# Kernel tuning notes

Measured on AMD Instinct MI355X. Metric: run time of the kernel, lower is better.

## Reference

```python
import jax, jax.numpy as jnp
import numpy as np

N, T, L = 4, 2048, 2048
DQIN, DFEAT, DQK, DV = 32, 34, 64, 64  # modality feat=34 -> V input = 34-2 = 32, K input = last col


def _sorted_timeline(k, shape):
    return jnp.sort(jax.random.uniform(k, shape, jnp.float32) * 100.0, axis=-1)


def setup_inputs() -> dict:
    key = jax.random.key(0)
    ks = jax.random.split(key, 32)
    inp = {}
    inp["ref_data"] = jax.random.normal(ks[0], (N, 1, T, DQIN), jnp.float32)
    inp["ref_t"] = _sorted_timeline(ks[1], (N, 1, T))
    inp["m1_data"] = jax.random.normal(ks[2], (N, 1, L, DFEAT), jnp.float32)
    inp["m1_t"] = _sorted_timeline(ks[3], (N, 1, L))
    inp["m2_data"] = jax.random.normal(ks[4], (N, 1, L, DFEAT), jnp.float32)
    inp["m2_t"] = _sorted_timeline(ks[5], (N, 1, L))
    inp["m3_data"] = jax.random.normal(ks[6], (N, 1, L, DFEAT), jnp.float32)
    inp["m3_t"] = _sorted_timeline(ks[7], (N, 1, L))
    # shared W_Q (bias=False): d_q_in -> d_qk
    inp["Wq"] = jax.random.normal(ks[8], (DQIN, DQK), jnp.float32) / np.sqrt(DQIN)
    # per-modality params: W_K: 1 -> d_qk (with bias), W_V: (DFEAT-2) -> d_v (with bias), log-temperature
    for i, m in enumerate(["1", "2", "3"]):
        b = 9 + 4 * i
        inp["Wk" + m] = jax.random.normal(ks[b], (1, DQK), jnp.float32)
        inp["bk" + m] = jax.random.normal(ks[b + 1], (DQK,), jnp.float32) * 0.02
        inp["Wv" + m] = jax.random.normal(ks[b + 2], (DFEAT - 2, DV), jnp.float32) / np.sqrt(DFEAT - 2)
        inp["bv" + m] = jax.random.normal(ks[b + 3], (DV,), jnp.float32) * 0.02
        inp["log_tau" + m] = jnp.zeros((), jnp.float32)  # log(init_tau=1)
    return inp


def _unimodal(Q, ref_t, data, t, Wk, bk, Wv, bv, log_tau):
    # K path: last feature column through linear, then feature_map_k = [1, -x]
    Kr = data[..., -1:] @ Wk + bk                                   # (N,1,L,DQK)
    K = jnp.concatenate([jnp.ones(Kr.shape[:-1] + (1,), Kr.dtype), -Kr], axis=-1)  # (N,1,L,DQK+1)
    V = data[..., :-2] @ Wv + bv                                    # (N,1,L,DV)
    tau = jnp.exp(log_tau)
    # gaussian weight: -(Q.K)^2 / tau
    S = -jnp.square(jnp.einsum('nhtc,nhlc->nhtl', Q, K)) / tau       # (N,1,T,L)
    mask = (ref_t[..., :, None] >= t[..., None, :]).astype(S.dtype)  # (N,1,T,L)
    A = jax.nn.softmax(S * mask, axis=-1) * mask
    return jnp.einsum('nhtl,nhlc->nhtc', A, V)                       # (N,1,T,DV)


def reference(ref_data, ref_t, m1_data, m1_t, m2_data, m2_t, m3_data, m3_t,
              Wq, Wk1, bk1, Wv1, bv1, log_tau1, Wk2, bk2, Wv2, bv2, log_tau2,
              Wk3, bk3, Wv3, bv3, log_tau3):
    # compute_Q (qk_type='time'): Q = add_one(W_Q(ref_data)) -> append ones column
    Qr = jnp.einsum('nhtd,dk->nhtk', ref_data, Wq)
    Q = jnp.concatenate([Qr, jnp.ones(Qr.shape[:-1] + (1,), Qr.dtype)], axis=-1)  # (N,1,T,DQK+1)
    y1 = _unimodal(Q, ref_t, m1_data, m1_t, Wk1, bk1, Wv1, bv1, log_tau1)
    y2 = _unimodal(Q, ref_t, m2_data, m2_t, Wk2, bk2, Wv2, bv2, log_tau2)
    y3 = _unimodal(Q, ref_t, m3_data, m3_t, Wk3, bk3, Wv3, bv3, log_tau3)
    # original returns dict {m1: y1, m2: y2, m3: y3}; stacked here (3,N,1,T,DV)
    return jnp.stack([y1, y2, y3], axis=0)
```

## Files before the change

kernel.cpp:

```cpp
#include <hip/hip_runtime.h>

namespace {

typedef unsigned int uint;
typedef unsigned short ushort_t;
typedef __attribute__((ext_vector_type(8))) short bf16x8;
typedef __attribute__((ext_vector_type(4))) float f32x4;

constexpr int N = 4, T = 2048, L = 2048;
constexpr int DQIN = 32, DQK = 64;

constexpr int VI_SZ = 3 * N * 64 * L;
constexpr int X_SZ = 3 * N * L;
constexpr int A_SZ = 3 * N * T;

union PK8 { int i[4]; bf16x8 s; };

__global__ __launch_bounds__(256) void mm_prep(
    const float* __restrict__ ref_data, const float* __restrict__ ref_t,
    const float* __restrict__ d1, const float* __restrict__ t1,
    const float* __restrict__ d2, const float* __restrict__ t2,
    const float* __restrict__ d3, const float* __restrict__ t3,
    const float* __restrict__ Wq,
    const float* __restrict__ Wk1, const float* __restrict__ bk1,
    const float* __restrict__ Wv1, const float* __restrict__ bv1, const float* __restrict__ lt1,
    const float* __restrict__ Wk2, const float* __restrict__ bk2,
    const float* __restrict__ Wv2, const float* __restrict__ bv2, const float* __restrict__ lt2,
    const float* __restrict__ Wk3, const float* __restrict__ bk3,
    const float* __restrict__ Wv3, const float* __restrict__ bv3, const float* __restrict__ lt3,
    float* __restrict__ Aq, float* __restrict__ Gq, int* __restrict__ Cq,
    ushort_t* __restrict__ VI, float* __restrict__ X) {
  const int b = blockIdx.x;
  const int tid = threadIdx.x;

  if (b < 96) {
    const int m = b >> 5;
    const int idx = (b & 31) * 256 + tid;
    __shared__ float sWq[DQIN * DQK];
    __shared__ float sWk[DQK];
    __shared__ float sbk[DQK];
    const float* Wk = (m == 0) ? Wk1 : (m == 1 ? Wk2 : Wk3);
    const float* bk = (m == 0) ? bk1 : (m == 1 ? bk2 : bk3);
    const float* lt = (m == 0) ? lt1 : (m == 1 ? lt2 : lt3);
    for (int i = tid; i < DQIN * DQK; i += 256) sWq[i] = Wq[i];
    if (tid < DQK) { sWk[tid] = Wk[tid]; sbk[tid] = bk[tid]; }
    __syncthreads();
    float x[DQIN];
    const float* rp = ref_data + idx * DQIN;
#pragma unroll
    for (int i = 0; i < DQIN; i++) x[i] = rp[i];
    float qr[DQK];
#pragma unroll
    for (int j = 0; j < DQK; j += 4) {
      float4 acc4 = make_float4(0.f, 0.f, 0.f, 0.f);
#pragma unroll
      for (int i = 0; i < DQIN; i++) {
        const float4 w = *(const float4*)&sWq[i * DQK + j];
        acc4.x = fmaf(x[i], w.x, acc4.x);
        acc4.y = fmaf(x[i], w.y, acc4.y);
        acc4.z = fmaf(x[i], w.z, acc4.z);
        acc4.w = fmaf(x[i], w.w, acc4.w);
      }
      qr[j] = acc4.x; qr[j + 1] = acc4.y; qr[j + 2] = acc4.z; qr[j + 3] = acc4.w;
    }
    const float rs = __expf(-0.5f * lt[0]);
    float g = 0.f, h = 0.f;
#pragma unroll
    for (int j = 1; j < DQK; j++) {
      g = fmaf(qr[j], sWk[j - 1], g);
      h = fmaf(qr[j], sbk[j - 1], h);
    }
    g += sWk[DQK - 1];
    h += sbk[DQK - 1];
    Aq[m * (N * T) + idx] = (qr[0] - h) * rs;
    Gq[m * (N * T) + idx] = g * rs;
  } else if (b < 192) {
    const int sidx = (b - 96) * 256 + tid;
    const int m = sidx >> 13;
    const int nt = sidx & 8191;
    const int n = nt >> 11;
    const float rt = ref_t[nt];
    const float* tml = ((m == 0) ? t1 : (m == 1 ? t2 : t3)) + n * L;
    int lo = 0, hi = L;
    while (lo < hi) {
      const int mid = (lo + hi) >> 1;
      if (tml[mid] <= rt) lo = mid + 1; else hi = mid;
    }
    Cq[m * 8192 + nt] = lo;
  } else {
    const int vb = b - 192;
    const int mn = vb >> 7;
    const int m = mn >> 2, n = mn & 3;
    const int lseg = (vb & 127) * 16;
    const float* dm = (m == 0) ? d1 : (m == 1 ? d2 : d3);
    const float* Wv = (m == 0) ? Wv1 : (m == 1 ? Wv2 : Wv3);
    const float* bv = (m == 0) ? bv1 : (m == 1 ? bv2 : bv3);
    const int cdim = tid & 63;
    const int qq = tid >> 6;
    const int l0 = lseg + qq * 4;

    float Wc[32];
#pragma unroll
    for (int i = 0; i < 32; i++) Wc[i] = Wv[i * 64 + cdim];
    const float bvc = bv[cdim];

    uint hi16[4], lo16[4];
#pragma unroll
    for (int k = 0; k < 4; k++) {
      const float* dp = dm + (size_t)(n * L + l0 + k) * 34;
      float acc = bvc;
#pragma unroll
      for (int i = 0; i < 32; i++) acc = fmaf(dp[i], Wc[i], acc);
      uint u = __float_as_uint(acc);
      uint h = (u + 0x7fffu + ((u >> 16) & 1u)) & 0xffff0000u;
      float res = acc - __uint_as_float(h);
      uint ul = __float_as_uint(res);
      uint hl = (ul + 0x7fffu + ((ul >> 16) & 1u)) >> 16;
      hi16[k] = h >> 16;
      lo16[k] = hl;
    }
    const int pkh0 = (int)(hi16[0] | (hi16[1] << 16));
    const int pkh1 = (int)(hi16[2] | (hi16[3] << 16));
    const int pkl0 = (int)(lo16[0] | (lo16[1] << 16));
    const int pkl1 = (int)(lo16[2] | (lo16[3] << 16));
    ushort_t* dst = VI + (size_t)(mn * 64 + cdim) * (2 * L) +
                    (l0 >> 3) * 16 + ((l0 >> 2) & 1) * 4;
    *(int2*)dst = make_int2(pkh0, pkh1);
    *(int2*)(dst + 8) = make_int2(pkl0, pkl1);

    if (tid < 16) {
      const int l = lseg + tid;
      X[mn * L + l] = dm[(size_t)(n * L + l) * 34 + 33];
    }
  }
}

__device__ inline void stage_chunk(ushort_t* dstbuf, const ushort_t* VIb, int ch,
                                   int w, int lane) {
#pragma unroll
  for (int i = 0; i < 8; i++) {
    const int n = (w * 8 + i) * 64 + lane;
    const int d = n >> 4;
    const int s = n & 15;
    const int u = (s - d) & 15;
    const ushort_t* src = VIb + (size_t)d * 4096 + ch * 128 + u * 8;
    __builtin_amdgcn_global_load_lds(
        (const __attribute__((address_space(1))) void*)src,
        (__attribute__((address_space(3))) void*)(dstbuf + n * 8),
        16, 0, 0);
  }
}

__global__ __launch_bounds__(128, 2) void mm_attn_main(
    const ushort_t* __restrict__ VI, const float* __restrict__ X,
    const float* __restrict__ Aq, const float* __restrict__ Gq, const int* __restrict__ Cq,
    float* __restrict__ out) {
  __shared__ ushort_t sbuf[2][8192];
  __shared__ float sx[2048];

  const int b = blockIdx.x;
  const int mn = b % 12;
  const int rg = 127 - (b / 12);

  const int tid = threadIdx.x;
  const int lane = tid & 63;
  const int w = tid >> 6;
  const int q = lane >> 4;
  const int m16 = lane & 15;

  const int tbase = mn * T + rg * 16;

  const int c = Cq[tbase + m16];
  const int cmax = __shfl(c, 15, 64);
  const int cmin = __shfl(c, 0, 64);
  const int nch = (cmax + 63) >> 6;

  const float a = Aq[tbase + m16];
  const float g = Gq[tbase + m16];

  f32x4 acc[4];
#pragma unroll
  for (int i = 0; i < 4; i++) acc[i] = (f32x4){0.f, 0.f, 0.f, 0.f};
  float z = 0.f;

  const ushort_t* VIb = VI + (size_t)(mn * 64) * 4096;
  const float* xg = X + mn * L;

  int oh[2][2], ol[2][2];
#pragma unroll
  for (int hh = 0; hh < 2; hh++) {
#pragma unroll
    for (int ct = 0; ct < 2; ct++) {
      const int d = hh * 32 + ct * 16 + m16;
      const int u0 = (w * 4 + q) * 2;
      oh[hh][ct] = d * 128 + (((u0 + 0) + d) & 15) * 8;
      ol[hh][ct] = d * 128 + (((u0 + 1) + d) & 15) * 8;
    }
  }

#pragma unroll
  for (int i = 0; i < 4; i++) {
    const float* src = xg + (i * 128 + tid) * 4;
    __builtin_amdgcn_global_load_lds(
        (const __attribute__((address_space(1))) void*)src,
        (__attribute__((address_space(3))) void*)(sx + (i * 128 + tid) * 4),
        16, 0, 0);
  }
  if (nch > 0) stage_chunk(sbuf[0], VIb, 0, w, lane);

  for (int ch = 0; ch < nch; ch++) {
    if (ch + 1 < nch) {
      stage_chunk(sbuf[(ch + 1) & 1], VIb, ch + 1, w, lane);
      asm volatile("s_waitcnt vmcnt(8)" ::: "memory");
    } else {
      asm volatile("s_waitcnt vmcnt(0)" ::: "memory");
    }
    asm volatile("" ::: "memory");
    __builtin_amdgcn_s_barrier();
    asm volatile("" ::: "memory");

    const int kbase = (ch << 6) + w * 32;
    if (kbase < cmax) {
      const int k0 = kbase + q * 8;
      const float4 xa = *(const float4*)&sx[k0];
      const float4 xb = *(const float4*)&sx[k0 + 4];
      const float xs[8] = {xa.x, xa.y, xa.z, xa.w, xb.x, xb.y, xb.z, xb.w};
      float wv[8];
      if (kbase + 32 <= cmin) {
#pragma unroll
        for (int jj = 0; jj < 8; jj++) {
          const float d = fmaf(-g, xs[jj], a);
          wv[jj] = __expf(-d * d);
          z += wv[jj];
        }
      } else {
#pragma unroll
        for (int jj = 0; jj < 8; jj++) {
          const float d = fmaf(-g, xs[jj], a);
          const float e = __expf(-d * d);
          wv[jj] = (k0 + jj < c) ? e : 0.f;
          z += wv[jj];
        }
      }
      PK8 ph, pl;
#pragma unroll
      for (int p2 = 0; p2 < 4; p2++) {
        const uint u0 = __float_as_uint(wv[2 * p2]);
        const uint u1 = __float_as_uint(wv[2 * p2 + 1]);
        const uint h0 = u0 & 0xffff0000u, h1 = u1 & 0xffff0000u;
        const float l0f = wv[2 * p2] - __uint_as_float(h0);
        const float l1f = wv[2 * p2 + 1] - __uint_as_float(h1);
        ph.i[p2] = (int)((h0 >> 16) | h1);
        pl.i[p2] = (int)((__float_as_uint(l0f) >> 16) | (__float_as_uint(l1f) & 0xffff0000u));
      }
      const bf16x8 ahi = ph.s, alo = pl.s;
      const ushort_t* buf = sbuf[ch & 1];
#pragma unroll
      for (int hh = 0; hh < 2; hh++) {
#pragma unroll
        for (int ct = 0; ct < 2; ct++) {
          const bf16x8 bh = *(const bf16x8*)(buf + oh[hh][ct]);
          const bf16x8 bl = *(const bf16x8*)(buf + ol[hh][ct]);
          acc[hh * 2 + ct] =
              __builtin_amdgcn_mfma_f32_16x16x32_bf16(ahi, bh, acc[hh * 2 + ct], 0, 0, 0);
          acc[hh * 2 + ct] =
              __builtin_amdgcn_mfma_f32_16x16x32_bf16(ahi, bl, acc[hh * 2 + ct], 0, 0, 0);
          acc[hh * 2 + ct] =
              __builtin_amdgcn_mfma_f32_16x16x32_bf16(alo, bh, acc[hh * 2 + ct], 0, 0, 0);
        }
      }
    }

    asm volatile("" ::: "memory");
    __builtin_amdgcn_s_barrier();
    asm volatile("" ::: "memory");
  }

  z += __shfl_xor(z, 16, 64);
  z += __shfl_xor(z, 32, 64);

  float* sc = (float*)sbuf;
  const int ow = w ^ 1;
#pragma unroll
  for (int p = 0; p < 2; p++)
    *(f32x4*)&sc[((w * 2 + p) * 64 + lane) * 4] = acc[ow * 2 + p];
  sc[1024 + w * 64 + lane] = z;
  __syncthreads();
  const float zt = z + sc[1024 + ow * 64 + lane];
  f32x4 r[2];
#pragma unroll
  for (int p = 0; p < 2; p++)
    r[p] = acc[w * 2 + p] + *(const f32x4*)&sc[((ow * 2 + p) * 64 + lane) * 4];

#pragma unroll
  for (int rr = 0; rr < 4; rr++) {
    const int row = q * 4 + rr;
    const float zr = __shfl(zt, row, 64);
    const int cr = __shfl(c, row, 64);
    const float inv = 1.0f / (zr + (float)(L - cr));
#pragma unroll
    for (int p = 0; p < 2; p++) {
      out[(size_t)(tbase + row) * 64 + w * 32 + p * 16 + m16] = r[p][rr] * inv;
    }
  }
}

}

extern "C" void kernel_launch(void* const* d_in, const int* in_sizes, int n_in,
                              void* d_out, int out_size, void* d_ws, size_t ws_size,
                              hipStream_t stream) {
  const float* ref_data = (const float*)d_in[0];
  const float* ref_t = (const float*)d_in[1];
  const float* m1_data = (const float*)d_in[2];
  const float* m1_t = (const float*)d_in[3];
  const float* m2_data = (const float*)d_in[4];
  const float* m2_t = (const float*)d_in[5];
  const float* m3_data = (const float*)d_in[6];
  const float* m3_t = (const float*)d_in[7];
  const float* Wq = (const float*)d_in[8];
  const float* Wk1 = (const float*)d_in[9];
  const float* bk1 = (const float*)d_in[10];
  const float* Wv1 = (const float*)d_in[11];
  const float* bv1 = (const float*)d_in[12];
  const float* lt1 = (const float*)d_in[13];
  const float* Wk2 = (const float*)d_in[14];
  const float* bk2 = (const float*)d_in[15];
  const float* Wv2 = (const float*)d_in[16];
  const float* bv2 = (const float*)d_in[17];
  const float* lt2 = (const float*)d_in[18];
  const float* Wk3 = (const float*)d_in[19];
  const float* bk3 = (const float*)d_in[20];
  const float* Wv3 = (const float*)d_in[21];
  const float* bv3 = (const float*)d_in[22];
  const float* lt3 = (const float*)d_in[23];

  float* ws = (float*)d_ws;
  ushort_t* VI = (ushort_t*)ws;
  float* Xw = ws + VI_SZ;
  float* Aq = Xw + X_SZ;
  float* Gq = Aq + A_SZ;
  int* Cq = (int*)(Gq + A_SZ);

  mm_prep<<<dim3(1728), dim3(256), 0, stream>>>(
      ref_data, ref_t, m1_data, m1_t, m2_data, m2_t, m3_data, m3_t, Wq,
      Wk1, bk1, Wv1, bv1, lt1, Wk2, bk2, Wv2, bv2, lt2, Wk3, bk3, Wv3, bv3, lt3,
      Aq, Gq, Cq, VI, Xw);
  mm_attn_main<<<dim3(12 * 128), dim3(128), 0, stream>>>(
      VI, Xw, Aq, Gq, Cq, (float*)d_out);
}
```

Measured before the change: 148.4 us.

## Process two 16-row query groups per block to share staged V chunks

Doubles the block to 256 threads so that two adjacent 16-row query groups share each LDS-staged V/K chunk. Staging work is split across four waves, which halves the global-to-LDS traffic per query row. The chunk count now follows the later group's causal limit, so the earlier group iterates over chunks it may not need (guarded by the kbase<cmax check). Launch bounds change to 256 threads with 3 blocks per CU, and the grid is halved.

```diff
diff --git a/kernel.cpp b/kernel.cpp
--- a/kernel.cpp
+++ b/kernel.cpp
@@ -136,10 +136,10 @@
 }
 
 __device__ inline void stage_chunk(ushort_t* dstbuf, const ushort_t* VIb, int ch,
-                                   int w, int lane) {
-#pragma unroll
-  for (int i = 0; i < 8; i++) {
-    const int n = (w * 8 + i) * 64 + lane;
+                                   int ww, int lane) {
+#pragma unroll
+  for (int i = 0; i < 4; i++) {
+    const int n = (ww * 4 + i) * 64 + lane;
     const int d = n >> 4;
     const int s = n & 15;
     const int u = (s - d) & 15;
@@ -151,7 +151,7 @@
   }
 }
 
-__global__ __launch_bounds__(128, 2) void mm_attn_main(
+__global__ __launch_bounds__(256, 3) void mm_attn_main(
     const ushort_t* __restrict__ VI, const float* __restrict__ X,
     const float* __restrict__ Aq, const float* __restrict__ Gq, const int* __restrict__ Cq,
     float* __restrict__ out) {
@@ -160,20 +160,24 @@
 
   const int b = blockIdx.x;
   const int mn = b % 12;
-  const int rg = 127 - (b / 12);
+  const int pj = 63 - (b / 12);
 
   const int tid = threadIdx.x;
   const int lane = tid & 63;
-  const int w = tid >> 6;
+  const int ww = tid >> 6;
+  const int rgl = ww >> 1;
+  const int w = ww & 1;
   const int q = lane >> 4;
   const int m16 = lane & 15;
 
-  const int tbase = mn * T + rg * 16;
+  const int tbase = mn * T + (pj * 2 + rgl) * 16;
 
   const int c = Cq[tbase + m16];
   const int cmax = __shfl(c, 15, 64);
   const int cmin = __shfl(c, 0, 64);
-  const int nch = (cmax + 63) >> 6;
+
+  const int cB = Cq[mn * T + (pj * 2 + 1) * 16 + 15];
+  const int nchB = (cB + 63) >> 6;
 
   const float a = Aq[tbase + m16];
   const float g = Gq[tbase + m16];
@@ -199,19 +203,20 @@
   }
 
 #pragma unroll
-  for (int i = 0; i < 4; i++) {
-    const float* src = xg + (i * 128 + tid) * 4;
+  for (int i = 0; i < 2; i++) {
+    const int unit = i * 256 + tid;
+    const float* src = xg + unit * 4;
     __builtin_amdgcn_global_load_lds(
         (const __attribute__((address_space(1))) void*)src,
-        (__attribute__((address_space(3))) void*)(sx + (i * 128 + tid) * 4),
+        (__attribute__((address_space(3))) void*)(sx + unit * 4),
         16, 0, 0);
   }
-  if (nch > 0) stage_chunk(sbuf[0], VIb, 0, w, lane);
-
-  for (int ch = 0; ch < nch; ch++) {
-    if (ch + 1 < nch) {
-      stage_chunk(sbuf[(ch + 1) & 1], VIb, ch + 1, w, lane);
-      asm volatile("s_waitcnt vmcnt(8)" ::: "memory");
+  if (nchB > 0) stage_chunk(sbuf[0], VIb, 0, ww, lane);
+
+  for (int ch = 0; ch < nchB; ch++) {
+    if (ch + 1 < nchB) {
+      stage_chunk(sbuf[(ch + 1) & 1], VIb, ch + 1, ww, lane);
+      asm volatile("s_waitcnt vmcnt(4)" ::: "memory");
     } else {
       asm volatile("s_waitcnt vmcnt(0)" ::: "memory");
     }
@@ -281,16 +286,17 @@
 
   float* sc = (float*)sbuf;
   const int ow = w ^ 1;
+  const int abase = rgl * 1024;
 #pragma unroll
   for (int p = 0; p < 2; p++)
-    *(f32x4*)&sc[((w * 2 + p) * 64 + lane) * 4] = acc[ow * 2 + p];
-  sc[1024 + w * 64 + lane] = z;
+    *(f32x4*)&sc[abase + ((w * 2 + p) * 64 + lane) * 4] = acc[ow * 2 + p];
+  sc[2048 + rgl * 128 + w * 64 + lane] = z;
   __syncthreads();
-  const float zt = z + sc[1024 + ow * 64 + lane];
+  const float zt = z + sc[2048 + rgl * 128 + ow * 64 + lane];
   f32x4 r[2];
 #pragma unroll
   for (int p = 0; p < 2; p++)
-    r[p] = acc[w * 2 + p] + *(const f32x4*)&sc[((ow * 2 + p) * 64 + lane) * 4];
+    r[p] = acc[w * 2 + p] + *(const f32x4*)&sc[abase + ((ow * 2 + p) * 64 + lane) * 4];
 
 #pragma unroll
   for (int rr = 0; rr < 4; rr++) {
@@ -346,6 +352,6 @@
       ref_data, ref_t, m1_data, m1_t, m2_data, m2_t, m3_data, m3_t, Wq,
       Wk1, bk1, Wv1, bv1, lt1, Wk2, bk2, Wv2, bv2, lt2, Wk3, bk3, Wv3, bv3, lt3,
       Aq, Gq, Cq, VI, Xw);
-  mm_attn_main<<<dim3(12 * 128), dim3(128), 0, stream>>>(
+  mm_attn_main<<<dim3(12 * 64), dim3(256), 0, stream>>>(
       VI, Xw, Aq, Gq, Cq, (float*)d_out);
 }
```

Measured after the change: 150.8 us. No clear change (+1.6%).
